# Kernel tuning notes

Hardware: AMD Instinct MI355X
Metric: run time of the kernel (lower is better)

## Reference

```python
import jax, jax.numpy as jnp
import numpy as np

B, N, E, H = 8, 1024, 768, 8
D = E // H  # 96

def setup_inputs() -> dict:
    key = jax.random.key(0)
    ks = jax.random.split(key, 5)
    s = 0.02
    return {
        "x": jax.random.normal(ks[0], (B, N, E), dtype=jnp.float32),
        "Wqkv": jax.random.normal(ks[1], (E, 3 * E), dtype=jnp.float32) * s,
        "bqkv": jax.random.normal(ks[2], (3 * E,), dtype=jnp.float32) * s,
        "Wproj": jax.random.normal(ks[3], (E, E), dtype=jnp.float32) * s,
        "bproj": jax.random.normal(ks[4], (E,), dtype=jnp.float32) * s,
    }

def reference(x, Wqkv, bqkv, Wproj, bproj):
    # qkv: [B,N,3E] -> split as (h d qkv), qkv fastest-varying -> [B,N,H,D,3]
    qkv = (x @ Wqkv + bqkv).reshape(B, N, H, D, 3)
    q = jnp.transpose(qkv[..., 0], (0, 2, 1, 3))  # [B,H,N,D]
    k = jnp.transpose(qkv[..., 1], (0, 2, 1, 3))
    v = jnp.transpose(qkv[..., 2], (0, 2, 1, 3))
    scale = E ** (-0.5)  # note: emb_size, not head_dim (faithful to source)
    scores = jnp.einsum('bhqd,bhkd->bhqk', q, k) * scale
    attn = jax.nn.softmax(scores, axis=-1)
    out = jnp.einsum('bhqk,bhkd->bhqd', attn, v)  # [B,H,N,D]
    out = jnp.transpose(out, (0, 2, 1, 3)).reshape(B, N, E)
    return out @ Wproj + bproj
```

## Files before the change

kernel.cpp:

```cpp
#include <hip/hip_runtime.h>

typedef unsigned short u16;
typedef __attribute__((ext_vector_type(8))) short short8;
typedef __attribute__((ext_vector_type(4))) short short4v;
typedef __attribute__((ext_vector_type(4))) float f32x4;
typedef __attribute__((ext_vector_type(2))) unsigned int uint2v;

#define DEV static __device__ __forceinline__

static_assert(sizeof(short8) == 16, "short8 must be 16B");

DEV u16 f2b(float f) {
  union { float f; unsigned u; } a; a.f = f;
  unsigned u = a.u;
  unsigned r = (u + 0x7FFFu + ((u >> 16) & 1u)) >> 16;
  return (u16)r;
}

DEV unsigned cvt_pk_bf16(float lo, float hi) {
  unsigned r;
  asm("v_cvt_pk_bf16_f32 %0, %1, %2" : "=v"(r) : "v"(lo), "v"(hi));
  return r;
}

DEV f32x4 mfma16(short8 a, short8 b, f32x4 c) {
  return __builtin_amdgcn_mfma_f32_16x16x32_bf16(a, b, c, 0, 0, 0);
}

DEV void gl_lds16(const u16* g, u16* l) {
  __builtin_amdgcn_global_load_lds(
      (const __attribute__((address_space(1))) void*)g,
      (__attribute__((address_space(3))) void*)l, 16, 0, 0);
}

constexpr int Bz = 8, Nseq = 1024, Emb = 768, Hh = 8, Dh = 96;
constexpr int Mrows = Bz * Nseq;
constexpr int K3 = 3 * Emb;
constexpr float QSCALE = 0.05205982021128899f;

__global__ __launch_bounds__(256) void k_cvt_x(const float* __restrict__ src,
                                               u16* __restrict__ dst) {
  int i = (blockIdx.x * 256 + threadIdx.x) * 4;
  float4 v = *(const float4*)(src + i);
  short4v o;
  o[0] = (short)f2b(v.x); o[1] = (short)f2b(v.y);
  o[2] = (short)f2b(v.z); o[3] = (short)f2b(v.w);
  *(short4v*)(dst + i) = o;
}

template <int PERM>
__global__ __launch_bounds__(256) void k_tcvt(const float* __restrict__ src,
                                              u16* __restrict__ dst, int R, int C) {
  __shared__ float t[32][33];
  int bx = blockIdx.x * 32;
  int by = blockIdx.y * 32;
  int c = threadIdx.x & 31, r8 = threadIdx.x >> 5;
#pragma unroll
  for (int p = 0; p < 4; ++p) {
    int r = r8 + p * 8;
    t[r][c] = src[(size_t)(by + r) * C + bx + c];
  }
  __syncthreads();
#pragma unroll
  for (int p = 0; p < 4; ++p) {
    int r = r8 + p * 8;
    int co = bx + r;
    int row = co;
    float mul = 1.f;
    if (PERM) {
      int h = co / 288, rem = co - h * 288;
      int d = rem / 3, s = rem - d * 3;
      row = s * 768 + h * 96 + d;
      if (s == 0) mul = QSCALE;
    }
    dst[(size_t)row * R + by + c] = f2b(t[c][r] * mul);
  }
}

__global__ __launch_bounds__(256) void k_permbias(const float* __restrict__ b,
                                                  float* __restrict__ bp) {
  int co = blockIdx.x * 256 + threadIdx.x;
  if (co < 2304) {
    int h = co / 288, rem = co - h * 288, d = rem / 3, s = rem - d * 3;
    bp[s * 768 + h * 96 + d] = b[co] * (s == 0 ? QSCALE : 1.f);
  }
}

template <int MODE>
__global__ __launch_bounds__(256, 2) void k_gemm_bt(
    const u16* __restrict__ A, const u16* __restrict__ Bt,
    const float* __restrict__ bias,
    u16* __restrict__ obf, u16* __restrict__ vtb, float* __restrict__ of32,
    int Nn, int Kdim) {
  __shared__ __align__(16) u16 Al[128 * 32];
  __shared__ __align__(16) u16 Bl[128 * 32];
  __shared__ __align__(16) u16 Cst[4][32 * 88];
  int m0 = blockIdx.x * 128, n0 = blockIdx.y * 128;
  int tid = threadIdx.x;
  int w = tid >> 6, l = tid & 63, lr = l >> 4, lc = l & 15;
  int wr = w >> 1, wc = w & 1;
  f32x4 acc[4][4] = {};
  int nkt = Kdim >> 5;
  for (int kt = 0; kt < nkt; ++kt) {
    __syncthreads();
#pragma unroll
    for (int i = 0; i < 2; ++i) {
      int idx = i * 256 + tid;
      int r = idx >> 2, c8 = (idx & 3) * 8;
      gl_lds16(A + (size_t)(m0 + r) * Kdim + kt * 32 + c8, &Al[idx * 8]);
      gl_lds16(Bt + (size_t)(n0 + r) * Kdim + kt * 32 + c8, &Bl[idx * 8]);
    }
    __syncthreads();
    short8 af[4];
#pragma unroll
    for (int mi = 0; mi < 4; ++mi)
      af[mi] = *(const short8*)&Al[(wr * 64 + mi * 16 + lc) * 32 + lr * 8];
#pragma unroll
    for (int ni = 0; ni < 4; ++ni) {
      short8 bf = *(const short8*)&Bl[(wc * 64 + ni * 16 + lc) * 32 + lr * 8];
#pragma unroll
      for (int mi = 0; mi < 4; ++mi)
        acc[mi][ni] = mfma16(af[mi], bf, acc[mi][ni]);
    }
  }

  if (MODE == 0) {
    if (n0 < 1536) {
      u16* Cb = &Cst[w][0];
#pragma unroll
      for (int mi2 = 0; mi2 < 2; ++mi2) {
#pragma unroll
        for (int mh = 0; mh < 2; ++mh) {
          int mi = mi2 * 2 + mh;
#pragma unroll
          for (int ni = 0; ni < 4; ++ni) {
            float bv = bias[n0 + wc * 64 + ni * 16 + lc];
#pragma unroll
            for (int r = 0; r < 4; ++r)
              Cb[(mh * 16 + lr * 4 + r) * 88 + ni * 16 + lc] =
                  f2b(acc[mi][ni][r] + bv);
          }
        }
#pragma unroll
        for (int i = 0; i < 4; ++i) {
          int idx = i * 64 + l;
          int row = idx >> 3, c8 = idx & 7;
          short8 vv = *(const short8*)&Cb[row * 88 + c8 * 8];
          int grow = m0 + wr * 64 + mi2 * 32 + row;
          int gcol = n0 + wc * 64 + c8 * 8;
          *(short8*)(obf + (size_t)grow * Nn + gcol) = vv;
        }
      }
    } else {
#pragma unroll
      for (int mi = 0; mi < 4; ++mi) {
#pragma unroll
        for (int ni = 0; ni < 4; ++ni) {
          int col = n0 + wc * 64 + ni * 16 + lc;
          float bv = bias[col];
          int dall = col - 1536;
          int row0 = m0 + wr * 64 + mi * 16 + lr * 4;
          short4v o4;
#pragma unroll
          for (int r = 0; r < 4; ++r) o4[r] = (short)f2b(acc[mi][ni][r] + bv);
          *(short4v*)(vtb + ((size_t)(row0 >> 10) * 768 + dall) * 1024 +
                      (row0 & 1023)) = o4;
        }
      }
    }
  } else {
#pragma unroll
    for (int mi = 0; mi < 4; ++mi) {
#pragma unroll
      for (int ni = 0; ni < 4; ++ni) {
        int col = n0 + wc * 64 + ni * 16 + lc;
        float bv = bias[col];
        int row0 = m0 + wr * 64 + mi * 16 + lr * 4;
#pragma unroll
        for (int r = 0; r < 4; ++r)
          of32[(size_t)(row0 + r) * Nn + col] = acc[mi][ni][r] + bv;
      }
    }
  }
}

__global__ __launch_bounds__(256, 3) void k_attn(const u16* __restrict__ qkvp,
                                                 const u16* __restrict__ vt,
                                                 u16* __restrict__ ctx) {
  __shared__ __align__(16) u16 smem[21504];
  int blk = blockIdx.x;
  int b = blk & 7, h = (blk >> 3) & 7, qt = blk >> 6;
  int tid = threadIdx.x, w = tid >> 6, l = tid & 63;
  int lr = l >> 4, lc = l & 15;
  int q0 = qt * 128 + w * 32;
  const u16* qptr = qkvp + (size_t)b * 1024 * 2304 + h * 96;
  const u16* kptr = qptr + 768;
  const u16* vtp  = vt + (size_t)(b * 768 + h * 96) * 1024 +
                    (size_t)lc * 1024 + lr * 8;
  u16* Pw = smem + 12288 + w * 2304;

  int soff[3], doff[3];
#pragma unroll
  for (int i = 0; i < 3; ++i) {
    int idx = i * 256 + tid;
    soff[i] = (idx / 12) * 2304 + (idx % 12) * 8;
    doff[i] = idx * 8;
  }

  short8 qf[2][3];
#pragma unroll
  for (int qi = 0; qi < 2; ++qi)
#pragma unroll
    for (int kf = 0; kf < 3; ++kf)
      qf[qi][kf] = *(const short8*)(qptr + (size_t)(q0 + qi * 16 + lc) * 2304 +
                                    kf * 32 + lr * 8);

  float mrow[2] = {-INFINITY, -INFINITY}, lrow[2] = {0.f, 0.f};
  f32x4 oacc[2][6] = {};

#pragma unroll
  for (int i = 0; i < 3; ++i) gl_lds16(kptr + soff[i], smem + doff[i]);
  __syncthreads();

  for (int kt = 0; kt < 16; ++kt) {
    const u16* Kc = smem + (kt & 1) * 6144;
    const u16* vkt = vtp + kt * 64;

    short8 va[6];
#pragma unroll
    for (int nf = 0; nf < 6; ++nf)
      va[nf] = *(const short8*)(vkt + (size_t)nf * 16 * 1024);

    if (kt < 15) {
      const u16* kg = kptr + (size_t)(kt + 1) * 64 * 2304;
      u16* db = smem + ((kt + 1) & 1) * 6144;
#pragma unroll
      for (int i = 0; i < 3; ++i) gl_lds16(kg + soff[i], db + doff[i]);
    }

    f32x4 sacc[2][4] = {};
    __builtin_amdgcn_s_setprio(1);
#pragma unroll
    for (int kfr = 0; kfr < 4; ++kfr) {
#pragma unroll
      for (int kf = 0; kf < 3; ++kf) {
        short8 kb = *(const short8*)&Kc[(kfr * 16 + lc) * 96 + kf * 32 + lr * 8];
        sacc[0][kfr] = mfma16(kb, qf[0][kf], sacc[0][kfr]);
        sacc[1][kfr] = mfma16(kb, qf[1][kf], sacc[1][kfr]);
      }
    }
    __builtin_amdgcn_s_setprio(0);

#pragma unroll
    for (int qi = 0; qi < 2; ++qi) {
      float mx = sacc[qi][0][0];
#pragma unroll
      for (int kfr = 0; kfr < 4; ++kfr)
#pragma unroll
        for (int r = 0; r < 4; ++r)
          if (kfr | r) mx = fmaxf(mx, sacc[qi][kfr][r]);
      mx = fmaxf(mx, __shfl_xor(mx, 16));
      mx = fmaxf(mx, __shfl_xor(mx, 32));
      if (__any(mx > mrow[qi] + 8.f)) {
        float nm = fmaxf(mrow[qi], mx);
        float sc = exp2f(mrow[qi] - nm);
        mrow[qi] = nm;
        lrow[qi] *= sc;
#pragma unroll
        for (int nf = 0; nf < 6; ++nf)
#pragma unroll
          for (int r = 0; r < 4; ++r) oacc[qi][nf][r] *= sc;
      }
      float m = mrow[qi], rs = 0.f;
#pragma unroll
      for (int kfr = 0; kfr < 4; ++kfr) {
        float p0 = exp2f(sacc[qi][kfr][0] - m);
        float p1 = exp2f(sacc[qi][kfr][1] - m);
        float p2 = exp2f(sacc[qi][kfr][2] - m);
        float p3 = exp2f(sacc[qi][kfr][3] - m);
        rs += (p0 + p1) + (p2 + p3);
        uint2v pk;
        pk[0] = cvt_pk_bf16(p0, p1);
        pk[1] = cvt_pk_bf16(p2, p3);
        *(uint2v*)&Pw[(qi * 16 + lc) * 72 + kfr * 16 + lr * 4] = pk;
      }
      rs += __shfl_xor(rs, 16);
      rs += __shfl_xor(rs, 32);
      lrow[qi] += rs;
    }
    asm volatile("s_waitcnt lgkmcnt(0)" ::: "memory");

    short8 pb0 = *(const short8*)&Pw[lc * 72 + lr * 8];
    short8 pb1 = *(const short8*)&Pw[(16 + lc) * 72 + lr * 8];
    short8 vc[6];
#pragma unroll
    for (int nf = 0; nf < 6; ++nf)
      vc[nf] = *(const short8*)(vkt + (size_t)nf * 16 * 1024 + 32);

    __builtin_amdgcn_s_setprio(1);
#pragma unroll
    for (int nf = 0; nf < 6; ++nf) {
      oacc[0][nf] = mfma16(va[nf], pb0, oacc[0][nf]);
      oacc[1][nf] = mfma16(va[nf], pb1, oacc[1][nf]);
    }
    __builtin_amdgcn_s_setprio(0);

    pb0 = *(const short8*)&Pw[lc * 72 + 32 + lr * 8];
    pb1 = *(const short8*)&Pw[(16 + lc) * 72 + 32 + lr * 8];
    __builtin_amdgcn_s_setprio(1);
#pragma unroll
    for (int nf = 0; nf < 6; ++nf) {
      oacc[0][nf] = mfma16(vc[nf], pb0, oacc[0][nf]);
      oacc[1][nf] = mfma16(vc[nf], pb1, oacc[1][nf]);
    }
    __builtin_amdgcn_s_setprio(0);
    __syncthreads();
  }

  u16* Cw = smem + w * 3328;
  float inv[2] = {1.0f / lrow[0], 1.0f / lrow[1]};
#pragma unroll
  for (int qi = 0; qi < 2; ++qi) {
#pragma unroll
    for (int nf = 0; nf < 6; ++nf) {
      uint2v pk;
      pk[0] = cvt_pk_bf16(oacc[qi][nf][0] * inv[qi], oacc[qi][nf][1] * inv[qi]);
      pk[1] = cvt_pk_bf16(oacc[qi][nf][2] * inv[qi], oacc[qi][nf][3] * inv[qi]);
      *(uint2v*)&Cw[(qi * 16 + lc) * 104 + nf * 16 + lr * 4] = pk;
    }
  }
  asm volatile("s_waitcnt lgkmcnt(0)" ::: "memory");
  int crow0 = b * 1024 + qt * 128 + w * 32;
#pragma unroll
  for (int i = 0; i < 6; ++i) {
    int idx = i * 64 + l;
    int row = idx / 12, c8 = idx % 12;
    short8 vv = *(const short8*)&Cw[row * 104 + c8 * 8];
    *(short8*)(ctx + (size_t)(crow0 + row) * 768 + h * 96 + c8 * 8) = vv;
  }
}

extern "C" void kernel_launch(void* const* d_in, const int* in_sizes, int n_in,
                              void* d_out, int out_size, void* d_ws, size_t ws_size,
                              hipStream_t stream) {
  const float* x     = (const float*)d_in[0];
  const float* Wqkv  = (const float*)d_in[1];
  const float* bqkv  = (const float*)d_in[2];
  const float* Wproj = (const float*)d_in[3];
  const float* bproj = (const float*)d_in[4];
  float* out = (float*)d_out;

  char* ws = (char*)d_ws;
  u16*   xb     = (u16*)(ws);
  u16*   wqkvT  = (u16*)(ws + 12582912);
  u16*   wprojT = (u16*)(ws + 16121856);
  float* bqkvp  = (float*)(ws + 17301504);
  u16*   qkvp   = (u16*)(ws + 17310720);
  u16*   vtb    = (u16*)(ws + 55059456);
  u16*   ctx    = xb;

  k_cvt_x<<<6144, 256, 0, stream>>>(x, xb);
  k_tcvt<1><<<dim3(K3 / 32, Emb / 32), 256, 0, stream>>>(Wqkv, wqkvT, Emb, K3);
  k_tcvt<0><<<dim3(Emb / 32, Emb / 32), 256, 0, stream>>>(Wproj, wprojT, Emb, Emb);
  k_permbias<<<9, 256, 0, stream>>>(bqkv, bqkvp);
  k_gemm_bt<0><<<dim3(Mrows / 128, K3 / 128), 256, 0, stream>>>(
      xb, wqkvT, bqkvp, qkvp, vtb, nullptr, K3, Emb);
  k_attn<<<512, 256, 0, stream>>>(qkvp, vtb, ctx);
  k_gemm_bt<1><<<dim3(Mrows / 128, Emb / 128), 256, 0, stream>>>(
      ctx, wprojT, bproj, nullptr, nullptr, out, Emb, Emb);
}
```

Measured before the change: 148.8 us.

## Load K tiles directly into registers with double-buffered prefetch, drop shared K staging

The attention kernel no longer stages K tiles in shared memory through async global-to-LDS copies and a per-tile block barrier. Each wave now loads its K fragments straight from global memory into two register buffers, prefetching the next tile while computing the current one, and also prefetches the next V fragment during the PV matmul. This removes the __syncthreads per key tile and the LDS round trip for K. In exchange it uses many more VGPRs, so launch bounds drop from 3 to 2 blocks per CU, and each wave issues redundant global loads of K that were previously shared across the four waves.

Result: slower. 187.6 us (+26.0%).

```diff
diff --git a/kernel.cpp b/kernel.cpp
--- a/kernel.cpp
+++ b/kernel.cpp
@@ -184,28 +184,123 @@
   }
 }
 
-__global__ __launch_bounds__(256, 3) void k_attn(const u16* __restrict__ qkvp,
+struct AttnState {
+  const u16* kln;
+  const u16* vln;
+  u16* Pw;
+  int lr, lc;
+};
+
+DEV void attn_body(int kt, const AttnState& st, const short8 (&qf)[2][3],
+                   short8 (&KC)[12], short8 (&KN)[12], short8 (&va)[6],
+                   float (&mrow)[2], float (&lrow)[2], f32x4 (&oacc)[2][6]) {
+  const int lr = st.lr, lc = st.lc;
+  f32x4 sacc[2][4] = {};
+  __builtin_amdgcn_s_setprio(1);
+#pragma unroll
+  for (int kfr = 0; kfr < 4; ++kfr) {
+#pragma unroll
+    for (int kf = 0; kf < 3; ++kf) {
+      sacc[0][kfr] = mfma16(KC[kfr * 3 + kf], qf[0][kf], sacc[0][kfr]);
+      sacc[1][kfr] = mfma16(KC[kfr * 3 + kf], qf[1][kf], sacc[1][kfr]);
+    }
+  }
+  __builtin_amdgcn_s_setprio(0);
+
+  short8 vc[6];
+#pragma unroll
+  for (int nf = 0; nf < 6; ++nf)
+    vc[nf] = *(const short8*)(st.vln + (size_t)nf * 16384 + kt * 64 + 32);
+  if (kt < 15) {
+#pragma unroll
+    for (int kfr = 0; kfr < 4; ++kfr)
+#pragma unroll
+      for (int kf = 0; kf < 3; ++kf)
+        KN[kfr * 3 + kf] = *(const short8*)(
+            st.kln + (size_t)((kt + 1) * 64 + kfr * 16) * 2304 + kf * 32);
+  }
+
+#pragma unroll
+  for (int qi = 0; qi < 2; ++qi) {
+    float mx = sacc[qi][0][0];
+#pragma unroll
+    for (int kfr = 0; kfr < 4; ++kfr)
+#pragma unroll
+      for (int r = 0; r < 4; ++r)
+        if (kfr | r) mx = fmaxf(mx, sacc[qi][kfr][r]);
+    mx = fmaxf(mx, __shfl_xor(mx, 16));
+    mx = fmaxf(mx, __shfl_xor(mx, 32));
+    if (__any(mx > mrow[qi] + 8.f)) {
+      float nm = fmaxf(mrow[qi], mx);
+      float sc = exp2f(mrow[qi] - nm);
+      mrow[qi] = nm;
+      lrow[qi] *= sc;
+#pragma unroll
+      for (int nf = 0; nf < 6; ++nf)
+#pragma unroll
+        for (int r = 0; r < 4; ++r) oacc[qi][nf][r] *= sc;
+    }
+    float m = mrow[qi], rs = 0.f;
+#pragma unroll
+    for (int kfr = 0; kfr < 4; ++kfr) {
+      float p0 = exp2f(sacc[qi][kfr][0] - m);
+      float p1 = exp2f(sacc[qi][kfr][1] - m);
+      float p2 = exp2f(sacc[qi][kfr][2] - m);
+      float p3 = exp2f(sacc[qi][kfr][3] - m);
+      rs += (p0 + p1) + (p2 + p3);
+      uint2v pk;
+      pk[0] = cvt_pk_bf16(p0, p1);
+      pk[1] = cvt_pk_bf16(p2, p3);
+      *(uint2v*)&st.Pw[(qi * 16 + lc) * 72 + kfr * 16 + lr * 4] = pk;
+    }
+    rs += __shfl_xor(rs, 16);
+    rs += __shfl_xor(rs, 32);
+    lrow[qi] += rs;
+  }
+  asm volatile("s_waitcnt lgkmcnt(0)" ::: "memory");
+
+  short8 pb0 = *(const short8*)&st.Pw[lc * 72 + lr * 8];
+  short8 pb1 = *(const short8*)&st.Pw[(16 + lc) * 72 + lr * 8];
+  __builtin_amdgcn_s_setprio(1);
+#pragma unroll
+  for (int nf = 0; nf < 6; ++nf) {
+    oacc[0][nf] = mfma16(va[nf], pb0, oacc[0][nf]);
+    oacc[1][nf] = mfma16(va[nf], pb1, oacc[1][nf]);
+  }
+  __builtin_amdgcn_s_setprio(0);
+  if (kt < 15) {
+#pragma unroll
+    for (int nf = 0; nf < 6; ++nf)
+      va[nf] = *(const short8*)(st.vln + (size_t)nf * 16384 + (kt + 1) * 64);
+  }
+  pb0 = *(const short8*)&st.Pw[lc * 72 + 32 + lr * 8];
+  pb1 = *(const short8*)&st.Pw[(16 + lc) * 72 + 32 + lr * 8];
+  __builtin_amdgcn_s_setprio(1);
+#pragma unroll
+  for (int nf = 0; nf < 6; ++nf) {
+    oacc[0][nf] = mfma16(vc[nf], pb0, oacc[0][nf]);
+    oacc[1][nf] = mfma16(vc[nf], pb1, oacc[1][nf]);
+  }
+  __builtin_amdgcn_s_setprio(0);
+}
+
+__global__ __launch_bounds__(256, 2) void k_attn(const u16* __restrict__ qkvp,
                                                  const u16* __restrict__ vt,
                                                  u16* __restrict__ ctx) {
-  __shared__ __align__(16) u16 smem[21504];
+  __shared__ __align__(16) u16 Pl[4][32 * 72];
+  __shared__ __align__(16) u16 Cst[4][32 * 104];
   int blk = blockIdx.x;
   int b = blk & 7, h = (blk >> 3) & 7, qt = blk >> 6;
   int tid = threadIdx.x, w = tid >> 6, l = tid & 63;
   int lr = l >> 4, lc = l & 15;
   int q0 = qt * 128 + w * 32;
   const u16* qptr = qkvp + (size_t)b * 1024 * 2304 + h * 96;
-  const u16* kptr = qptr + 768;
-  const u16* vtp  = vt + (size_t)(b * 768 + h * 96) * 1024 +
-                    (size_t)lc * 1024 + lr * 8;
-  u16* Pw = smem + 12288 + w * 2304;
-
-  int soff[3], doff[3];
-#pragma unroll
-  for (int i = 0; i < 3; ++i) {
-    int idx = i * 256 + tid;
-    soff[i] = (idx / 12) * 2304 + (idx % 12) * 8;
-    doff[i] = idx * 8;
-  }
+
+  AttnState st;
+  st.kln = qptr + 768 + (size_t)lc * 2304 + lr * 8;
+  st.vln = vt + (size_t)(b * 768 + h * 96) * 1024 + (size_t)lc * 1024 + lr * 8;
+  st.Pw = Pl[w];
+  st.lr = lr; st.lc = lc;
 
   short8 qf[2][3];
 #pragma unroll
@@ -218,106 +313,23 @@
   float mrow[2] = {-INFINITY, -INFINITY}, lrow[2] = {0.f, 0.f};
   f32x4 oacc[2][6] = {};
 
-#pragma unroll
-  for (int i = 0; i < 3; ++i) gl_lds16(kptr + soff[i], smem + doff[i]);
-  __syncthreads();
-
-  for (int kt = 0; kt < 16; ++kt) {
-    const u16* Kc = smem + (kt & 1) * 6144;
-    const u16* vkt = vtp + kt * 64;
-
-    short8 va[6];
-#pragma unroll
-    for (int nf = 0; nf < 6; ++nf)
-      va[nf] = *(const short8*)(vkt + (size_t)nf * 16 * 1024);
-
-    if (kt < 15) {
-      const u16* kg = kptr + (size_t)(kt + 1) * 64 * 2304;
-      u16* db = smem + ((kt + 1) & 1) * 6144;
-#pragma unroll
-      for (int i = 0; i < 3; ++i) gl_lds16(kg + soff[i], db + doff[i]);
-    }
-
-    f32x4 sacc[2][4] = {};
-    __builtin_amdgcn_s_setprio(1);
-#pragma unroll
-    for (int kfr = 0; kfr < 4; ++kfr) {
-#pragma unroll
-      for (int kf = 0; kf < 3; ++kf) {
-        short8 kb = *(const short8*)&Kc[(kfr * 16 + lc) * 96 + kf * 32 + lr * 8];
-        sacc[0][kfr] = mfma16(kb, qf[0][kf], sacc[0][kfr]);
-        sacc[1][kfr] = mfma16(kb, qf[1][kf], sacc[1][kfr]);
-      }
-    }
-    __builtin_amdgcn_s_setprio(0);
-
-#pragma unroll
-    for (int qi = 0; qi < 2; ++qi) {
-      float mx = sacc[qi][0][0];
-#pragma unroll
-      for (int kfr = 0; kfr < 4; ++kfr)
-#pragma unroll
-        for (int r = 0; r < 4; ++r)
-          if (kfr | r) mx = fmaxf(mx, sacc[qi][kfr][r]);
-      mx = fmaxf(mx, __shfl_xor(mx, 16));
-      mx = fmaxf(mx, __shfl_xor(mx, 32));
-      if (__any(mx > mrow[qi] + 8.f)) {
-        float nm = fmaxf(mrow[qi], mx);
-        float sc = exp2f(mrow[qi] - nm);
-        mrow[qi] = nm;
-        lrow[qi] *= sc;
-#pragma unroll
-        for (int nf = 0; nf < 6; ++nf)
-#pragma unroll
-          for (int r = 0; r < 4; ++r) oacc[qi][nf][r] *= sc;
-      }
-      float m = mrow[qi], rs = 0.f;
-#pragma unroll
-      for (int kfr = 0; kfr < 4; ++kfr) {
-        float p0 = exp2f(sacc[qi][kfr][0] - m);
-        float p1 = exp2f(sacc[qi][kfr][1] - m);
-        float p2 = exp2f(sacc[qi][kfr][2] - m);
-        float p3 = exp2f(sacc[qi][kfr][3] - m);
-        rs += (p0 + p1) + (p2 + p3);
-        uint2v pk;
-        pk[0] = cvt_pk_bf16(p0, p1);
-        pk[1] = cvt_pk_bf16(p2, p3);
-        *(uint2v*)&Pw[(qi * 16 + lc) * 72 + kfr * 16 + lr * 4] = pk;
-      }
-      rs += __shfl_xor(rs, 16);
-      rs += __shfl_xor(rs, 32);
-      lrow[qi] += rs;
-    }
-    asm volatile("s_waitcnt lgkmcnt(0)" ::: "memory");
-
-    short8 pb0 = *(const short8*)&Pw[lc * 72 + lr * 8];
-    short8 pb1 = *(const short8*)&Pw[(16 + lc) * 72 + lr * 8];
-    short8 vc[6];
-#pragma unroll
-    for (int nf = 0; nf < 6; ++nf)
-      vc[nf] = *(const short8*)(vkt + (size_t)nf * 16 * 1024 + 32);
-
-    __builtin_amdgcn_s_setprio(1);
-#pragma unroll
-    for (int nf = 0; nf < 6; ++nf) {
-      oacc[0][nf] = mfma16(va[nf], pb0, oacc[0][nf]);
-      oacc[1][nf] = mfma16(va[nf], pb1, oacc[1][nf]);
-    }
-    __builtin_amdgcn_s_setprio(0);
-
-    pb0 = *(const short8*)&Pw[lc * 72 + 32 + lr * 8];
-    pb1 = *(const short8*)&Pw[(16 + lc) * 72 + 32 + lr * 8];
-    __builtin_amdgcn_s_setprio(1);
-#pragma unroll
-    for (int nf = 0; nf < 6; ++nf) {
-      oacc[0][nf] = mfma16(vc[nf], pb0, oacc[0][nf]);
-      oacc[1][nf] = mfma16(vc[nf], pb1, oacc[1][nf]);
-    }
-    __builtin_amdgcn_s_setprio(0);
-    __syncthreads();
-  }
-
-  u16* Cw = smem + w * 3328;
+  short8 kA[12], kB[12], va[6];
+#pragma unroll
+  for (int kfr = 0; kfr < 4; ++kfr)
+#pragma unroll
+    for (int kf = 0; kf < 3; ++kf)
+      kA[kfr * 3 + kf] = *(const short8*)(st.kln + (size_t)(kfr * 16) * 2304 +
+                                          kf * 32);
+#pragma unroll
+  for (int nf = 0; nf < 6; ++nf)
+    va[nf] = *(const short8*)(st.vln + (size_t)nf * 16384);
+
+  for (int kt2 = 0; kt2 < 16; kt2 += 2) {
+    attn_body(kt2,     st, qf, kA, kB, va, mrow, lrow, oacc);
+    attn_body(kt2 + 1, st, qf, kB, kA, va, mrow, lrow, oacc);
+  }
+
+  u16* Cw = Cst[w];
   float inv[2] = {1.0f / lrow[0], 1.0f / lrow[1]};
 #pragma unroll
   for (int qi = 0; qi < 2; ++qi) {
```

## Triple-buffer GEMM LDS staging and hoist all V loads early in attention

Applied to the files above, without the earlier changes.

The bf16 GEMM kernel now keeps three LDS buffers and prefetches tiles two K-steps ahead, using explicit vmcnt waits plus a single barrier per iteration in place of two __syncthreads. The epilogue staging buffer reuses the same shared allocation. In the attention kernel, both halves of the V fragments are loaded at the top of each iteration so global latency overlaps the QK and softmax work. Attention occupancy is dropped from 3 to 2 blocks per CU to make room for the extra live registers, which costs latency hiding through waves.

After: 133.2 us, median of 5. 10.5% less time.

```diff
diff --git a/kernel.cpp b/kernel.cpp
--- a/kernel.cpp
+++ b/kernel.cpp
@@ -92,41 +92,55 @@
     const float* __restrict__ bias,
     u16* __restrict__ obf, u16* __restrict__ vtb, float* __restrict__ of32,
     int Nn, int Kdim) {
-  __shared__ __align__(16) u16 Al[128 * 32];
-  __shared__ __align__(16) u16 Bl[128 * 32];
-  __shared__ __align__(16) u16 Cst[4][32 * 88];
+  __shared__ __align__(16) u16 smem[24576];
   int m0 = blockIdx.x * 128, n0 = blockIdx.y * 128;
   int tid = threadIdx.x;
   int w = tid >> 6, l = tid & 63, lr = l >> 4, lc = l & 15;
   int wr = w >> 1, wc = w & 1;
   f32x4 acc[4][4] = {};
   int nkt = Kdim >> 5;
-  for (int kt = 0; kt < nkt; ++kt) {
-    __syncthreads();
+
+  auto stage = [&](u16* bA, u16* bB, int t) {
 #pragma unroll
     for (int i = 0; i < 2; ++i) {
       int idx = i * 256 + tid;
-      int r = idx >> 2, c8 = (idx & 3) * 8;
-      gl_lds16(A + (size_t)(m0 + r) * Kdim + kt * 32 + c8, &Al[idx * 8]);
-      gl_lds16(Bt + (size_t)(n0 + r) * Kdim + kt * 32 + c8, &Bl[idx * 8]);
-    }
-    __syncthreads();
+      int rr = idx >> 2, cc = (idx & 3) * 8;
+      gl_lds16(A + (size_t)(m0 + rr) * Kdim + t * 32 + cc, bA + idx * 8);
+      gl_lds16(Bt + (size_t)(n0 + rr) * Kdim + t * 32 + cc, bB + idx * 8);
+    }
+  };
+
+  u16 *a0 = smem, *a1 = smem + 4096, *a2 = smem + 8192;
+  u16 *b0 = smem + 12288, *b1 = smem + 16384, *b2 = smem + 20480;
+  stage(a0, b0, 0);
+  stage(a1, b1, 1);
+
+  for (int kt = 0; kt < nkt; ++kt) {
+    if (kt < nkt - 1)
+      asm volatile("s_waitcnt vmcnt(4) lgkmcnt(0)\n\ts_barrier" ::: "memory");
+    else
+      asm volatile("s_waitcnt vmcnt(0) lgkmcnt(0)\n\ts_barrier" ::: "memory");
+    if (kt + 2 < nkt) stage(a2, b2, kt + 2);
     short8 af[4];
 #pragma unroll
     for (int mi = 0; mi < 4; ++mi)
-      af[mi] = *(const short8*)&Al[(wr * 64 + mi * 16 + lc) * 32 + lr * 8];
+      af[mi] = *(const short8*)&a0[(wr * 64 + mi * 16 + lc) * 32 + lr * 8];
 #pragma unroll
     for (int ni = 0; ni < 4; ++ni) {
-      short8 bf = *(const short8*)&Bl[(wc * 64 + ni * 16 + lc) * 32 + lr * 8];
+      short8 bf = *(const short8*)&b0[(wc * 64 + ni * 16 + lc) * 32 + lr * 8];
 #pragma unroll
       for (int mi = 0; mi < 4; ++mi)
         acc[mi][ni] = mfma16(af[mi], bf, acc[mi][ni]);
     }
-  }
+    u16* t;
+    t = a0; a0 = a1; a1 = a2; a2 = t;
+    t = b0; b0 = b1; b1 = b2; b2 = t;
+  }
+  __syncthreads();
 
   if (MODE == 0) {
     if (n0 < 1536) {
-      u16* Cb = &Cst[w][0];
+      u16* Cb = smem + w * 2816;
 #pragma unroll
       for (int mi2 = 0; mi2 < 2; ++mi2) {
 #pragma unroll
@@ -184,7 +198,7 @@
   }
 }
 
-__global__ __launch_bounds__(256, 3) void k_attn(const u16* __restrict__ qkvp,
+__global__ __launch_bounds__(256, 2) void k_attn(const u16* __restrict__ qkvp,
                                                  const u16* __restrict__ vt,
                                                  u16* __restrict__ ctx) {
   __shared__ __align__(16) u16 smem[21504];
@@ -226,10 +240,13 @@
     const u16* Kc = smem + (kt & 1) * 6144;
     const u16* vkt = vtp + kt * 64;
 
-    short8 va[6];
-#pragma unroll
-    for (int nf = 0; nf < 6; ++nf)
-      va[nf] = *(const short8*)(vkt + (size_t)nf * 16 * 1024);
+    short8 va[6], vc[6];
+#pragma unroll
+    for (int nf = 0; nf < 6; ++nf) {
+      va[nf] = *(const short8*)(vkt + (size_t)nf * 16384);
+      vc[nf] = *(const short8*)(vkt + (size_t)nf * 16384 + 32);
+    }
+    asm volatile("" ::: "memory");
 
     if (kt < 15) {
       const u16* kg = kptr + (size_t)(kt + 1) * 64 * 2304;
@@ -292,11 +309,6 @@
 
     short8 pb0 = *(const short8*)&Pw[lc * 72 + lr * 8];
     short8 pb1 = *(const short8*)&Pw[(16 + lc) * 72 + lr * 8];
-    short8 vc[6];
-#pragma unroll
-    for (int nf = 0; nf < 6; ++nf)
-      vc[nf] = *(const short8*)(vkt + (size_t)nf * 16 * 1024 + 32);
-
     __builtin_amdgcn_s_setprio(1);
 #pragma unroll
     for (int nf = 0; nf < 6; ++nf) {
```
